# Optimization experiments

Measured on AMD Instinct MI355X. Metric: run time of the kernel, lower is better.

## Reference

```python
import jax, jax.numpy as jnp
import numpy as np

B, T, D = 2, 2048, 4096
H, KH, HD = 32, 8, 128          # n_heads, n_kv_heads, head_dim = D // H
WINDOW, NGLOBAL = 1024, 32      # sliding window size, global sink tokens
ROPE_BASE = 500000.0


def _rope_tables(seq_len, dim):
    inv_freq = 1.0 / (ROPE_BASE ** (np.arange(0, dim, 2, dtype=np.float64) / dim))
    freqs = np.outer(np.arange(seq_len, dtype=np.float64), inv_freq)
    emb = np.concatenate([freqs, freqs], axis=-1)  # [T, HD]
    cos = jnp.asarray(np.cos(emb), dtype=jnp.float32)[None, None]  # [1,1,T,HD]
    sin = jnp.asarray(np.sin(emb), dtype=jnp.float32)[None, None]
    return cos, sin


def _window_global_mask(seq_len, window, n_global):
    i = np.arange(seq_len)[:, None]  # query pos
    j = np.arange(seq_len)[None, :]  # key pos
    causal = j <= i
    local = j > (i - window)
    global_keys = j < n_global
    return jnp.asarray(causal & (local | global_keys))[None, None]  # [1,1,T,T] bool


def rotate_half(x):
    x1, x2 = jnp.split(x, 2, axis=-1)
    return jnp.concatenate([-x2, x1], axis=-1)


def setup_inputs() -> dict:
    key = jax.random.key(0)
    kx, kq, kk, kv, ko = jax.random.split(key, 5)
    s = 1.0 / np.sqrt(D)
    x = jax.random.normal(kx, (B, T, D), dtype=jnp.float32)
    # Linear weights stored [in, out] (y = x @ W), same math as torch's x @ W.T
    Wq = jax.random.normal(kq, (D, H * HD), dtype=jnp.float32) * s
    Wk = jax.random.normal(kk, (D, KH * HD), dtype=jnp.float32) * s
    Wv = jax.random.normal(kv, (D, KH * HD), dtype=jnp.float32) * s
    Wo = jax.random.normal(ko, (H * HD, D), dtype=jnp.float32) * s
    cos, sin = _rope_tables(T, HD)
    mask = _window_global_mask(T, WINDOW, NGLOBAL)
    return {"x": x, "Wq": Wq, "Wk": Wk, "Wv": Wv, "Wo": Wo,
            "cos": cos, "sin": sin, "mask": mask}


def reference(x, Wq, Wk, Wv, Wo, cos, sin, mask):
    Bx, Tx, Dx = x.shape
    q = (x @ Wq).reshape(Bx, Tx, H, HD).transpose(0, 2, 1, 3)   # [B,H,T,HD]
    k = (x @ Wk).reshape(Bx, Tx, KH, HD).transpose(0, 2, 1, 3)  # [B,KH,T,HD]
    v = (x @ Wv).reshape(Bx, Tx, KH, HD).transpose(0, 2, 1, 3)
    # RoPE
    q = q * cos + rotate_half(q) * sin
    k = k * cos + rotate_half(k) * sin
    # GQA: repeat_interleave KV heads to match query heads (faithful to source)
    factor = H // KH
    k = jnp.repeat(k, factor, axis=1)  # [B,H,T,HD]
    v = jnp.repeat(v, factor, axis=1)
    # SDPA with dense bool mask (True = attend), default scale 1/sqrt(HD)
    scale = 1.0 / np.sqrt(HD)
    scores = jnp.einsum('bhqd,bhkd->bhqk', q, k) * scale  # [B,H,T,T]
    scores = jnp.where(mask, scores, jnp.finfo(scores.dtype).min)
    attn = jax.nn.softmax(scores, axis=-1)
    out = jnp.einsum('bhqk,bhkd->bhqd', attn, v)
    out = out.transpose(0, 2, 1, 3).reshape(Bx, Tx, H * HD)
    return out @ Wo
```

## Files before the change

kernel.cpp:

```cpp
#include <hip/hip_runtime.h>
#include <stdint.h>

typedef unsigned short u16;
typedef __bf16 bf16x8 __attribute__((ext_vector_type(8)));
typedef float f32x4 __attribute__((ext_vector_type(4)));

#define D_MODEL 4096
#define T_SEQ   2048
#define B_SZ    2
#define NH      32
#define NKV     8
#define HDIM    128
#define WINDOW  1024
#define NGLOB   32
#define QSTR    6144

static constexpr float SCALE = 0.08838834764831845f;

__device__ __forceinline__ u16 f2b(float f) {
  __bf16 h = (__bf16)f;
  return __builtin_bit_cast(u16, h);
}
__device__ __forceinline__ float b2f(u16 u) {
  return (float)__builtin_bit_cast(__bf16, u);
}

__global__ __launch_bounds__(256) void convert_bf16_kernel(const float* __restrict__ in,
                                                           u16* __restrict__ outp, int n4) {
  int i = blockIdx.x * 256 + threadIdx.x;
  if (i >= n4) return;
  float4 v = ((const float4*)in)[i];
  ushort4 o;
  o.x = f2b(v.x); o.y = f2b(v.y); o.z = f2b(v.z); o.w = f2b(v.w);
  ((ushort4*)outp)[i] = o;
}

__global__ __launch_bounds__(256) void transpose_w_kernel(const float* __restrict__ W,
                                                          u16* __restrict__ Wt, int Kd, int Nd) {
  __shared__ float tile[32][33];
  int tx = threadIdx.x & 31, ty = threadIdx.x >> 5;
  int bx = blockIdx.x * 32;
  int by = blockIdx.y * 32;
#pragma unroll
  for (int i = 0; i < 4; ++i)
    tile[ty + i * 8][tx] = W[(size_t)(by + ty + i * 8) * Nd + bx + tx];
  __syncthreads();
#pragma unroll
  for (int i = 0; i < 4; ++i)
    Wt[(size_t)(bx + ty + i * 8) * Kd + by + tx] = f2b(tile[tx][ty + i * 8]);
}

__global__ __launch_bounds__(256) void transpose_v_kernel(const u16* __restrict__ in,
                                                          u16* __restrict__ outp) {
  __shared__ u16 tile[32][33];
  int tx = threadIdx.x & 31, ty = threadIdx.x >> 5;
  int x0 = blockIdx.x * 32;
  int t0 = blockIdx.y * 32;
  int b = blockIdx.z;
  const u16* src = in + (size_t)b * T_SEQ * QSTR;
  u16* dst = outp + (size_t)b * (NKV * HDIM) * T_SEQ;
#pragma unroll
  for (int i = 0; i < 4; ++i)
    tile[ty + i * 8][tx] = src[(size_t)(t0 + ty + i * 8) * QSTR + x0 + tx];
  __syncthreads();
#pragma unroll
  for (int i = 0; i < 4; ++i)
    dst[(size_t)(x0 + ty + i * 8) * T_SEQ + t0 + tx] = tile[tx][ty + i * 8];
}

template <typename CT>
__global__ __launch_bounds__(512, 2) void gemm256_kernel(const u16* __restrict__ A,
                                                         const u16* __restrict__ Bt,
                                                         CT* __restrict__ C,
                                                         int ldc, int K) {
  __shared__ u16 sh[65536];
  const int tid = threadIdx.x;
  const int wave = tid >> 6, lane = tid & 63;
  const int g = lane >> 4, li = lane & 15;
  const int wr = wave >> 2, wc = wave & 3;
  const int m0 = blockIdx.y * 256, n0 = blockIdx.x * 256;
  const int r0 = tid >> 3;
  const int cs = ((tid & 7) ^ ((tid >> 3) & 7)) << 3;
  const u16* pA = A + (size_t)(m0 + r0) * K + cs;
  const u16* pB = Bt + (size_t)(n0 + r0) * K + cs;
  const int sl0 = (g ^ (li & 7)) << 3;
  const int sl1 = ((4 + g) ^ (li & 7)) << 3;
  const int nT = K >> 6;

  f32x4 acc[8][4];
  f32x4 zz = {0.f, 0.f, 0.f, 0.f};
#pragma unroll
  for (int M = 0; M < 8; ++M)
#pragma unroll
    for (int n = 0; n < 4; ++n) acc[M][n] = zz;

  auto stage = [&](const u16* src0, int ts, int dstBase) {
#pragma unroll
    for (int i = 0; i < 2; ++i) {
      const u16* s = src0 + (size_t)(i * 64) * K + ts * 64;
      __builtin_amdgcn_global_load_lds((__attribute__((address_space(1))) void*)s,
                                       (__attribute__((address_space(3))) void*)(sh + dstBase + i * 4096 + wave * 512),
                                       16, 0, 0);
    }
  };

  stage(pA, 0, 0);
  stage(pA + (size_t)128 * K, 0, 8192);
  stage(pB, 0, 16384);
  stage(pB + (size_t)128 * K, 0, 24576);
  stage(pB, 1, 32768 + 16384);
  stage(pB + (size_t)128 * K, 1, 32768 + 24576);
  stage(pA, 1, 32768);
  asm volatile("s_waitcnt vmcnt(6)" ::: "memory");
  __builtin_amdgcn_s_barrier();

  bf16x8 afr[4][2], bfr[4][2];
  for (int t = 0; t < nT; ++t) {
    const int cur = t & 1;
    const int ab = cur * 32768, bb = ab + 16384;
    const int nb = (cur ^ 1) * 32768;
    const int tn1 = (t + 1 < nT) ? t + 1 : nT - 1;
    const int tn2 = (t + 2 < nT) ? t + 2 : nT - 1;
#pragma unroll
    for (int n = 0; n < 4; ++n) {
      int row = wc * 64 + n * 16 + li;
      bfr[n][0] = *(const bf16x8*)&sh[bb + row * 64 + sl0];
      bfr[n][1] = *(const bf16x8*)&sh[bb + row * 64 + sl1];
    }
#pragma unroll
    for (int m = 0; m < 4; ++m) {
      int row = wr * 128 + m * 16 + li;
      afr[m][0] = *(const bf16x8*)&sh[ab + row * 64 + sl0];
      afr[m][1] = *(const bf16x8*)&sh[ab + row * 64 + sl1];
    }
    stage(pA + (size_t)128 * K, tn1, nb + 8192);
    __builtin_amdgcn_s_barrier();
    asm volatile("s_waitcnt lgkmcnt(0)" ::: "memory");
    __builtin_amdgcn_sched_barrier(0);
    __builtin_amdgcn_s_setprio(1);
#pragma unroll
    for (int m = 0; m < 4; ++m)
#pragma unroll
      for (int n = 0; n < 2; ++n) {
        acc[m][n] = __builtin_amdgcn_mfma_f32_16x16x32_bf16(afr[m][0], bfr[n][0], acc[m][n], 0, 0, 0);
        acc[m][n] = __builtin_amdgcn_mfma_f32_16x16x32_bf16(afr[m][1], bfr[n][1], acc[m][n], 0, 0, 0);
      }
    __builtin_amdgcn_s_setprio(0);
    __builtin_amdgcn_s_barrier();
    stage(pB, tn2, bb);
    __builtin_amdgcn_s_barrier();
    __builtin_amdgcn_s_setprio(1);
#pragma unroll
    for (int m = 0; m < 4; ++m)
#pragma unroll
      for (int n = 2; n < 4; ++n) {
        acc[m][n] = __builtin_amdgcn_mfma_f32_16x16x32_bf16(afr[m][0], bfr[n][0], acc[m][n], 0, 0, 0);
        acc[m][n] = __builtin_amdgcn_mfma_f32_16x16x32_bf16(afr[m][1], bfr[n][1], acc[m][n], 0, 0, 0);
      }
    __builtin_amdgcn_s_setprio(0);
    __builtin_amdgcn_s_barrier();
#pragma unroll
    for (int m = 0; m < 4; ++m) {
      int row = wr * 128 + 64 + m * 16 + li;
      afr[m][0] = *(const bf16x8*)&sh[ab + row * 64 + sl0];
      afr[m][1] = *(const bf16x8*)&sh[ab + row * 64 + sl1];
    }
    stage(pB + (size_t)128 * K, tn2, bb + 8192);
    __builtin_amdgcn_s_barrier();
    asm volatile("s_waitcnt lgkmcnt(0)" ::: "memory");
    __builtin_amdgcn_sched_barrier(0);
    __builtin_amdgcn_s_setprio(1);
#pragma unroll
    for (int m = 0; m < 4; ++m)
#pragma unroll
      for (int n = 0; n < 2; ++n) {
        acc[4 + m][n] = __builtin_amdgcn_mfma_f32_16x16x32_bf16(afr[m][0], bfr[n][0], acc[4 + m][n], 0, 0, 0);
        acc[4 + m][n] = __builtin_amdgcn_mfma_f32_16x16x32_bf16(afr[m][1], bfr[n][1], acc[4 + m][n], 0, 0, 0);
      }
    __builtin_amdgcn_s_setprio(0);
    __builtin_amdgcn_s_barrier();
    stage(pA, tn2, ab);
    __builtin_amdgcn_s_barrier();
    __builtin_amdgcn_s_setprio(1);
#pragma unroll
    for (int m = 0; m < 4; ++m)
#pragma unroll
      for (int n = 2; n < 4; ++n) {
        acc[4 + m][n] = __builtin_amdgcn_mfma_f32_16x16x32_bf16(afr[m][0], bfr[n][0], acc[4 + m][n], 0, 0, 0);
        acc[4 + m][n] = __builtin_amdgcn_mfma_f32_16x16x32_bf16(afr[m][1], bfr[n][1], acc[4 + m][n], 0, 0, 0);
      }
    __builtin_amdgcn_s_setprio(0);
    asm volatile("s_waitcnt vmcnt(6)" ::: "memory");
    __builtin_amdgcn_s_barrier();
  }
#pragma unroll
  for (int M = 0; M < 8; ++M)
#pragma unroll
    for (int n = 0; n < 4; ++n)
#pragma unroll
      for (int r = 0; r < 4; ++r) {
        int row = m0 + wr * 128 + M * 16 + g * 4 + r;
        int col = n0 + wc * 64 + n * 16 + li;
        if constexpr (sizeof(CT) == 2)
          C[(size_t)row * ldc + col] = (CT)f2b(acc[M][n][r]);
        else
          C[(size_t)row * ldc + col] = acc[M][n][r];
      }
}

__global__ __launch_bounds__(512, 2) void gemm192_kernel(const u16* __restrict__ A,
                                                         const u16* __restrict__ Bt,
                                                         u16* __restrict__ C,
                                                         int ldc, int K) {
  __shared__ u16 sh[57344];
  const int tid = threadIdx.x;
  const int wave = tid >> 6, lane = tid & 63;
  const int g = lane >> 4, li = lane & 15;
  const int wr = wave >> 2, wc = wave & 3;
  const int m0 = blockIdx.y * 256, n0 = blockIdx.x * 192;
  const int r0 = tid >> 3;
  const int cs = ((tid & 7) ^ ((tid >> 3) & 7)) << 3;
  const u16* pA = A + (size_t)(m0 + r0) * K + cs;
  const u16* pB = Bt + (size_t)(n0 + r0) * K + cs;
  const int sl0 = (g ^ (li & 7)) << 3;
  const int sl1 = ((4 + g) ^ (li & 7)) << 3;
  const int nT = K >> 6;

  f32x4 acc[8][3];
  f32x4 zz = {0.f, 0.f, 0.f, 0.f};
#pragma unroll
  for (int M = 0; M < 8; ++M)
#pragma unroll
    for (int n = 0; n < 3; ++n) acc[M][n] = zz;

  auto stage64 = [&](const u16* src0, int ts, int dstU16) {
    __builtin_amdgcn_global_load_lds(
        (__attribute__((address_space(1))) void*)(src0 + (size_t)ts * 64),
        (__attribute__((address_space(3))) void*)(sh + dstU16 + wave * 512), 16, 0, 0);
  };

#pragma unroll
  for (int u = 0; u < 4; ++u) stage64(pA + (size_t)(u * 64) * K, 0, u * 4096);
#pragma unroll
  for (int u = 0; u < 3; ++u) stage64(pB + (size_t)(u * 64) * K, 0, 16384 + u * 4096);
#pragma unroll
  for (int u = 0; u < 4; ++u) stage64(pA + (size_t)(u * 64) * K, 1, 28672 + u * 4096);
#pragma unroll
  for (int u = 0; u < 3; ++u) stage64(pB + (size_t)(u * 64) * K, 1, 28672 + 16384 + u * 4096);
  asm volatile("s_waitcnt vmcnt(7)" ::: "memory");
  __builtin_amdgcn_s_barrier();

  bf16x8 afr[4][2], bfr[3][2];
  for (int t = 0; t < nT; ++t) {
    const int ab = (t & 1) * 28672, bb = ab + 16384;
    const int tn2 = (t + 2 < nT) ? t + 2 : nT - 1;
#pragma unroll
    for (int n = 0; n < 3; ++n) {
      int row = wc * 48 + n * 16 + li;
      bfr[n][0] = *(const bf16x8*)&sh[bb + row * 64 + sl0];
      bfr[n][1] = *(const bf16x8*)&sh[bb + row * 64 + sl1];
    }
#pragma unroll
    for (int m = 0; m < 4; ++m) {
      int row = wr * 128 + m * 16 + li;
      afr[m][0] = *(const bf16x8*)&sh[ab + row * 64 + sl0];
      afr[m][1] = *(const bf16x8*)&sh[ab + row * 64 + sl1];
    }
    __builtin_amdgcn_s_barrier();
    asm volatile("s_waitcnt lgkmcnt(0)" ::: "memory");
    __builtin_amdgcn_sched_barrier(0);
    __builtin_amdgcn_s_setprio(1);
#pragma unroll
    for (int m = 0; m < 4; ++m)
#pragma unroll
      for (int n = 0; n < 2; ++n) {
        acc[m][n] = __builtin_amdgcn_mfma_f32_16x16x32_bf16(afr[m][0], bfr[n][0], acc[m][n], 0, 0, 0);
        acc[m][n] = __builtin_amdgcn_mfma_f32_16x16x32_bf16(afr[m][1], bfr[n][1], acc[m][n], 0, 0, 0);
      }
    __builtin_amdgcn_s_setprio(0);
    __builtin_amdgcn_s_barrier();
    stage64(pB, tn2, bb);
    stage64(pB + (size_t)64 * K, tn2, bb + 4096);
    stage64(pA, tn2, ab);
    __builtin_amdgcn_s_barrier();
    __builtin_amdgcn_s_setprio(1);
#pragma unroll
    for (int m = 0; m < 4; ++m) {
      acc[m][2] = __builtin_amdgcn_mfma_f32_16x16x32_bf16(afr[m][0], bfr[2][0], acc[m][2], 0, 0, 0);
      acc[m][2] = __builtin_amdgcn_mfma_f32_16x16x32_bf16(afr[m][1], bfr[2][1], acc[m][2], 0, 0, 0);
    }
    __builtin_amdgcn_s_setprio(0);
    __builtin_amdgcn_s_barrier();
#pragma unroll
    for (int m = 0; m < 4; ++m) {
      int row = wr * 128 + 64 + m * 16 + li;
      afr[m][0] = *(const bf16x8*)&sh[ab + row * 64 + sl0];
      afr[m][1] = *(const bf16x8*)&sh[ab + row * 64 + sl1];
    }
    stage64(pB + (size_t)128 * K, tn2, bb + 8192);
    stage64(pA + (size_t)128 * K, tn2, ab + 8192);
    __builtin_amdgcn_s_barrier();
    asm volatile("s_waitcnt lgkmcnt(0)" ::: "memory");
    __builtin_amdgcn_sched_barrier(0);
    __builtin_amdgcn_s_setprio(1);
#pragma unroll
    for (int m = 0; m < 4; ++m)
#pragma unroll
      for (int n = 0; n < 2; ++n) {
        acc[4 + m][n] = __builtin_amdgcn_mfma_f32_16x16x32_bf16(afr[m][0], bfr[n][0], acc[4 + m][n], 0, 0, 0);
        acc[4 + m][n] = __builtin_amdgcn_mfma_f32_16x16x32_bf16(afr[m][1], bfr[n][1], acc[4 + m][n], 0, 0, 0);
      }
    __builtin_amdgcn_s_setprio(0);
    __builtin_amdgcn_s_barrier();
    stage64(pA + (size_t)64 * K, tn2, ab + 4096);
    stage64(pA + (size_t)192 * K, tn2, ab + 12288);
    __builtin_amdgcn_s_barrier();
    __builtin_amdgcn_s_setprio(1);
#pragma unroll
    for (int m = 0; m < 4; ++m) {
      acc[4 + m][2] = __builtin_amdgcn_mfma_f32_16x16x32_bf16(afr[m][0], bfr[2][0], acc[4 + m][2], 0, 0, 0);
      acc[4 + m][2] = __builtin_amdgcn_mfma_f32_16x16x32_bf16(afr[m][1], bfr[2][1], acc[4 + m][2], 0, 0, 0);
    }
    __builtin_amdgcn_s_setprio(0);
    asm volatile("s_waitcnt vmcnt(7)" ::: "memory");
    __builtin_amdgcn_s_barrier();
  }
#pragma unroll
  for (int M = 0; M < 8; ++M)
#pragma unroll
    for (int n = 0; n < 3; ++n)
#pragma unroll
      for (int r = 0; r < 4; ++r) {
        int row = m0 + wr * 128 + M * 16 + g * 4 + r;
        int col = n0 + wc * 48 + n * 16 + li;
        C[(size_t)row * ldc + col] = f2b(acc[M][n][r]);
      }
}

__global__ __launch_bounds__(256) void rope_kernel(u16* __restrict__ qkv,
                                                   const float* __restrict__ cosp,
                                                   const float* __restrict__ sinp) {
  int idx = blockIdx.x * 256 + threadIdx.x;
  int d8 = idx & 7;
  int rest = idx >> 3;
  int hh = rest % (NH + NKV);
  int bt = rest / (NH + NKV);
  if (bt >= B_SZ * T_SEQ) return;
  int tok = bt & (T_SEQ - 1);
  int d0 = d8 * 8;
  const float4* cp = (const float4*)(cosp + (size_t)tok * HDIM + d0);
  const float4* sp = (const float4*)(sinp + (size_t)tok * HDIM + d0);
  float4 cA = cp[0], cB = cp[1];
  float4 sA = sp[0], sB = sp[1];
  float cc[8] = {cA.x, cA.y, cA.z, cA.w, cB.x, cB.y, cB.z, cB.w};
  float ss[8] = {sA.x, sA.y, sA.z, sA.w, sB.x, sB.y, sB.z, sB.w};
  u16* base = qkv + (size_t)bt * QSTR + hh * HDIM;
  bf16x8 v1 = *(const bf16x8*)(base + d0);
  bf16x8 v2 = *(const bf16x8*)(base + d0 + 64);
  bf16x8 o1, o2;
#pragma unroll
  for (int j = 0; j < 8; ++j) {
    float xa = (float)v1[j], xb = (float)v2[j];
    o1[j] = (__bf16)(xa * cc[j] - xb * ss[j]);
    o2[j] = (__bf16)(xb * cc[j] + xa * ss[j]);
  }
  *(bf16x8*)(base + d0) = o1;
  *(bf16x8*)(base + d0 + 64) = o2;
}

__global__ __launch_bounds__(256) void attn_kernel(const u16* __restrict__ qp,
                                                   const u16* __restrict__ kp,
                                                   const u16* __restrict__ vtp,
                                                   u16* __restrict__ ctx) {
  __shared__ u16 Kt[64 * 128];
  __shared__ u16 Vt[128 * 64];
  __shared__ u16 Pl[4][16 * 64];
  int tid = threadIdx.x;
  int w = tid >> 6, lane = tid & 63;
  int g = lane >> 4, li = lane & 15;
  int i0 = blockIdx.x * 64;
  int h = blockIdx.y, b = blockIdx.z;
  int kh = h >> 2;
  f32x4 zz = {0.f, 0.f, 0.f, 0.f};

  bf16x8 qf[4];
  size_t qrow = (size_t)(b * T_SEQ + i0 + w * 16 + li) * QSTR + h * HDIM;
#pragma unroll
  for (int c = 0; c < 4; ++c) qf[c] = *(const bf16x8*)(qp + qrow + c * 32 + g * 8);

  f32x4 o[8];
#pragma unroll
  for (int f = 0; f < 8; ++f) o[f] = zz;
  float m_s[4] = {-1e30f, -1e30f, -1e30f, -1e30f};
  float l_s[4] = {0.f, 0.f, 0.f, 0.f};

  int jmax = i0 + 63;
  for (int j0 = 0; j0 <= jmax; j0 += 64) {
    if (!((j0 < NGLOB) || (j0 + 63 > i0 - WINDOW))) continue;
    __syncthreads();
#pragma unroll
    for (int i = 0; i < 4; ++i) {
      int o8 = tid + 256 * i;
      int krow = o8 >> 4, kch = o8 & 15;
      size_t gk = (size_t)(b * T_SEQ + j0 + krow) * QSTR + kh * HDIM + kch * 8;
      *(bf16x8*)&Kt[(krow * 128 + kch * 8) ^ ((krow & 7) << 3)] = *(const bf16x8*)(kp + gk);
      int vrow = o8 >> 3, vch = o8 & 7;
      size_t gv = ((size_t)(b * NKV + kh) * HDIM + vrow) * T_SEQ + j0 + vch * 8;
      *(bf16x8*)&Vt[(vrow * 64 + vch * 8) ^ ((vrow & 7) << 3)] = *(const bf16x8*)(vtp + gv);
    }
    __syncthreads();

    f32x4 s[4];
#pragma unroll
    for (int kb = 0; kb < 4; ++kb) s[kb] = zz;
#pragma unroll
    for (int c = 0; c < 4; ++c) {
      int hd0 = c * 32 + g * 8;
#pragma unroll
      for (int kb = 0; kb < 4; ++kb) {
        int key = kb * 16 + li;
        bf16x8 kf = *(const bf16x8*)&Kt[(key * 128 + hd0) ^ ((key & 7) << 3)];
        s[kb] = __builtin_amdgcn_mfma_f32_16x16x32_bf16(qf[c], kf, s[kb], 0, 0, 0);
      }
    }

    float corr[4];
#pragma unroll
    for (int r = 0; r < 4; ++r) {
      int irow = i0 + w * 16 + g * 4 + r;
      float x[4];
#pragma unroll
      for (int kb = 0; kb < 4; ++kb) {
        int j = j0 + kb * 16 + li;
        float xx = s[kb][r] * SCALE;
        bool vm = (j <= irow) && ((j > irow - WINDOW) || (j < NGLOB));
        x[kb] = vm ? xx : -1e30f;
      }
      float mt = fmaxf(fmaxf(x[0], x[1]), fmaxf(x[2], x[3]));
#pragma unroll
      for (int dd = 1; dd < 16; dd <<= 1) mt = fmaxf(mt, __shfl_xor(mt, dd, 64));
      float mn = fmaxf(m_s[r], mt);
      corr[r] = __expf(m_s[r] - mn);
      m_s[r] = mn;
      float rs = 0.f;
      int prow = g * 4 + r;
#pragma unroll
      for (int kb = 0; kb < 4; ++kb) {
        x[kb] = __expf(x[kb] - mn);
        rs += x[kb];
        Pl[w][(prow * 64 + kb * 16 + li) ^ ((prow & 7) << 3)] = f2b(x[kb]);
      }
#pragma unroll
      for (int dd = 1; dd < 16; dd <<= 1) rs += __shfl_xor(rs, dd, 64);
      l_s[r] = l_s[r] * corr[r] + rs;
    }
#pragma unroll
    for (int f = 0; f < 8; ++f) {
      o[f][0] *= corr[0]; o[f][1] *= corr[1];
      o[f][2] *= corr[2]; o[f][3] *= corr[3];
    }

    bf16x8 pa0 = *(const bf16x8*)&Pl[w][(li * 64 + 0 + g * 8) ^ ((li & 7) << 3)];
    bf16x8 pa1 = *(const bf16x8*)&Pl[w][(li * 64 + 32 + g * 8) ^ ((li & 7) << 3)];

#pragma unroll
    for (int f = 0; f < 8; ++f) {
      int hd = f * 16 + li;
      bf16x8 v0 = *(const bf16x8*)&Vt[(hd * 64 + 0 + g * 8) ^ ((li & 7) << 3)];
      bf16x8 v1 = *(const bf16x8*)&Vt[(hd * 64 + 32 + g * 8) ^ ((li & 7) << 3)];
      o[f] = __builtin_amdgcn_mfma_f32_16x16x32_bf16(pa0, v0, o[f], 0, 0, 0);
      o[f] = __builtin_amdgcn_mfma_f32_16x16x32_bf16(pa1, v1, o[f], 0, 0, 0);
    }
  }

#pragma unroll
  for (int f = 0; f < 8; ++f)
#pragma unroll
    for (int r = 0; r < 4; ++r) {
      size_t orow = (size_t)(b * T_SEQ + i0 + w * 16 + g * 4 + r) * (NH * HDIM) + h * HDIM + f * 16 + li;
      ctx[orow] = f2b(o[f][r] / l_s[r]);
    }
}

extern "C" void kernel_launch(void* const* d_in, const int* in_sizes, int n_in,
                              void* d_out, int out_size, void* d_ws, size_t ws_size,
                              hipStream_t stream) {
  const float* x    = (const float*)d_in[0];
  const float* Wq   = (const float*)d_in[1];
  const float* Wk   = (const float*)d_in[2];
  const float* Wv   = (const float*)d_in[3];
  const float* Wo   = (const float*)d_in[4];
  const float* cosp = (const float*)d_in[5];
  const float* sinp = (const float*)d_in[6];

  char* ws = (char*)d_ws;
  u16* xb     = (u16*)(ws + 0ull);
  u16* Wqkvt  = (u16*)(ws + 33554432ull);
  u16* Wot    = (u16*)(ws + 83886080ull);
  u16* qkv    = (u16*)(ws + 117440512ull);
  u16* ctx    = xb;
  u16* vT     = Wqkvt;

  convert_bf16_kernel<<<16384, 256, 0, stream>>>(x, xb, 4194304);
  transpose_w_kernel<<<dim3(128, 128), 256, 0, stream>>>(Wq, Wqkvt, 4096, 4096);
  transpose_w_kernel<<<dim3(32, 128), 256, 0, stream>>>(Wk, Wqkvt + (size_t)4096 * 4096, 4096, 1024);
  transpose_w_kernel<<<dim3(32, 128), 256, 0, stream>>>(Wv, Wqkvt + (size_t)5120 * 4096, 4096, 1024);
  transpose_w_kernel<<<dim3(128, 128), 256, 0, stream>>>(Wo, Wot, 4096, 4096);

  gemm192_kernel<<<dim3(32, 16), 512, 0, stream>>>(xb, Wqkvt, qkv, QSTR, 4096);

  transpose_v_kernel<<<dim3(32, 64, 2), 256, 0, stream>>>(qkv + 5120, vT);

  rope_kernel<<<5120, 256, 0, stream>>>(qkv, cosp, sinp);

  attn_kernel<<<dim3(32, 32, 2), 256, 0, stream>>>(qkv, qkv + 4096, vT, ctx);

  gemm256_kernel<float><<<dim3(16, 16), 512, 0, stream>>>(ctx, Wot, (float*)d_out, 4096, 4096);
}
```

Baseline: 577.4 us.

## Enlarge attention query tile, load K/V directly to LDS, transpose score MFMA

The attention block grows from 64 to 128 query rows with 8 waves, so each K/V tile staged in shared memory serves twice as many queries. K/V tiles are copied with global_load_lds direct-to-LDS transfers, with the swizzle moved into the global address. The QK^T MFMA operands are swapped so each lane owns one query row, which turns the row-max and row-sum reductions into two cross-group shuffles. The softmax scale is folded into Q during RoPE, which adds an extra bf16 rounding of scaled Q. Larger blocks cut the grid in half and may process more fully masked rows near the diagonal.

```diff
diff --git a/kernel.cpp b/kernel.cpp
--- a/kernel.cpp
+++ b/kernel.cpp
@@ -20,9 +20,6 @@
 __device__ __forceinline__ u16 f2b(float f) {
   __bf16 h = (__bf16)f;
   return __builtin_bit_cast(u16, h);
-}
-__device__ __forceinline__ float b2f(u16 u) {
-  return (float)__builtin_bit_cast(__bf16, u);
 }
 
 __global__ __launch_bounds__(256) void convert_bf16_kernel(const float* __restrict__ in,
@@ -354,6 +351,7 @@
   float4 sA = sp[0], sB = sp[1];
   float cc[8] = {cA.x, cA.y, cA.z, cA.w, cB.x, cB.y, cB.z, cB.w};
   float ss[8] = {sA.x, sA.y, sA.z, sA.w, sB.x, sB.y, sB.z, sB.w};
+  float scl = (hh < NH) ? SCALE : 1.0f;
   u16* base = qkv + (size_t)bt * QSTR + hh * HDIM;
   bf16x8 v1 = *(const bf16x8*)(base + d0);
   bf16x8 v2 = *(const bf16x8*)(base + d0 + 64);
@@ -361,24 +359,24 @@
 #pragma unroll
   for (int j = 0; j < 8; ++j) {
     float xa = (float)v1[j], xb = (float)v2[j];
-    o1[j] = (__bf16)(xa * cc[j] - xb * ss[j]);
-    o2[j] = (__bf16)(xb * cc[j] + xa * ss[j]);
+    o1[j] = (__bf16)((xa * cc[j] - xb * ss[j]) * scl);
+    o2[j] = (__bf16)((xb * cc[j] + xa * ss[j]) * scl);
   }
   *(bf16x8*)(base + d0) = o1;
   *(bf16x8*)(base + d0 + 64) = o2;
 }
 
-__global__ __launch_bounds__(256) void attn_kernel(const u16* __restrict__ qp,
+__global__ __launch_bounds__(512) void attn_kernel(const u16* __restrict__ qp,
                                                    const u16* __restrict__ kp,
                                                    const u16* __restrict__ vtp,
                                                    u16* __restrict__ ctx) {
   __shared__ u16 Kt[64 * 128];
   __shared__ u16 Vt[128 * 64];
-  __shared__ u16 Pl[4][16 * 64];
+  __shared__ u16 Pl[8][16 * 64];
   int tid = threadIdx.x;
   int w = tid >> 6, lane = tid & 63;
   int g = lane >> 4, li = lane & 15;
-  int i0 = blockIdx.x * 64;
+  int i0 = blockIdx.x * 128;
   int h = blockIdx.y, b = blockIdx.z;
   int kh = h >> 2;
   f32x4 zz = {0.f, 0.f, 0.f, 0.f};
@@ -391,22 +389,26 @@
   f32x4 o[8];
 #pragma unroll
   for (int f = 0; f < 8; ++f) o[f] = zz;
-  float m_s[4] = {-1e30f, -1e30f, -1e30f, -1e30f};
-  float l_s[4] = {0.f, 0.f, 0.f, 0.f};
-
-  int jmax = i0 + 63;
+  float m_s = -1e30f, l_s = 0.f;
+  const int irow = i0 + w * 16 + li;
+
+  int jmax = i0 + 127;
   for (int j0 = 0; j0 <= jmax; j0 += 64) {
     if (!((j0 < NGLOB) || (j0 + 63 > i0 - WINDOW))) continue;
     __syncthreads();
 #pragma unroll
-    for (int i = 0; i < 4; ++i) {
-      int o8 = tid + 256 * i;
+    for (int i = 0; i < 2; ++i) {
+      int o8 = tid + 512 * i;
       int krow = o8 >> 4, kch = o8 & 15;
-      size_t gk = (size_t)(b * T_SEQ + j0 + krow) * QSTR + kh * HDIM + kch * 8;
-      *(bf16x8*)&Kt[(krow * 128 + kch * 8) ^ ((krow & 7) << 3)] = *(const bf16x8*)(kp + gk);
+      size_t gk = (size_t)(b * T_SEQ + j0 + krow) * QSTR + kh * HDIM + (kch ^ (krow & 7)) * 8;
+      __builtin_amdgcn_global_load_lds((__attribute__((address_space(1))) void*)(kp + gk),
+                                       (__attribute__((address_space(3))) void*)(Kt + o8 * 8),
+                                       16, 0, 0);
       int vrow = o8 >> 3, vch = o8 & 7;
-      size_t gv = ((size_t)(b * NKV + kh) * HDIM + vrow) * T_SEQ + j0 + vch * 8;
-      *(bf16x8*)&Vt[(vrow * 64 + vch * 8) ^ ((vrow & 7) << 3)] = *(const bf16x8*)(vtp + gv);
+      size_t gv = ((size_t)(b * NKV + kh) * HDIM + vrow) * T_SEQ + j0 + (vch ^ (vrow & 7)) * 8;
+      __builtin_amdgcn_global_load_lds((__attribute__((address_space(1))) void*)(vtp + gv),
+                                       (__attribute__((address_space(3))) void*)(Vt + o8 * 8),
+                                       16, 0, 0);
     }
     __syncthreads();
 
@@ -420,44 +422,50 @@
       for (int kb = 0; kb < 4; ++kb) {
         int key = kb * 16 + li;
         bf16x8 kf = *(const bf16x8*)&Kt[(key * 128 + hd0) ^ ((key & 7) << 3)];
-        s[kb] = __builtin_amdgcn_mfma_f32_16x16x32_bf16(qf[c], kf, s[kb], 0, 0, 0);
-      }
-    }
-
-    float corr[4];
-#pragma unroll
-    for (int r = 0; r < 4; ++r) {
-      int irow = i0 + w * 16 + g * 4 + r;
-      float x[4];
-#pragma unroll
-      for (int kb = 0; kb < 4; ++kb) {
-        int j = j0 + kb * 16 + li;
-        float xx = s[kb][r] * SCALE;
+        s[kb] = __builtin_amdgcn_mfma_f32_16x16x32_bf16(kf, qf[c], s[kb], 0, 0, 0);
+      }
+    }
+
+    float x[4][4];
+    float mt = -1e30f;
+#pragma unroll
+    for (int kb = 0; kb < 4; ++kb)
+#pragma unroll
+      for (int r = 0; r < 4; ++r) {
+        int j = j0 + kb * 16 + g * 4 + r;
         bool vm = (j <= irow) && ((j > irow - WINDOW) || (j < NGLOB));
-        x[kb] = vm ? xx : -1e30f;
-      }
-      float mt = fmaxf(fmaxf(x[0], x[1]), fmaxf(x[2], x[3]));
-#pragma unroll
-      for (int dd = 1; dd < 16; dd <<= 1) mt = fmaxf(mt, __shfl_xor(mt, dd, 64));
-      float mn = fmaxf(m_s[r], mt);
-      corr[r] = __expf(m_s[r] - mn);
-      m_s[r] = mn;
-      float rs = 0.f;
-      int prow = g * 4 + r;
-#pragma unroll
-      for (int kb = 0; kb < 4; ++kb) {
-        x[kb] = __expf(x[kb] - mn);
-        rs += x[kb];
-        Pl[w][(prow * 64 + kb * 16 + li) ^ ((prow & 7) << 3)] = f2b(x[kb]);
-      }
-#pragma unroll
-      for (int dd = 1; dd < 16; dd <<= 1) rs += __shfl_xor(rs, dd, 64);
-      l_s[r] = l_s[r] * corr[r] + rs;
-    }
+        float xx = vm ? s[kb][r] : -1e30f;
+        x[kb][r] = xx;
+        mt = fmaxf(mt, xx);
+      }
+    mt = fmaxf(mt, __shfl_xor(mt, 16, 64));
+    mt = fmaxf(mt, __shfl_xor(mt, 32, 64));
+    float mn = fmaxf(m_s, mt);
+    float corr = __expf(m_s - mn);
+    m_s = mn;
+    float rs = 0.f;
+#pragma unroll
+    for (int kb = 0; kb < 4; ++kb) {
+      ushort4 pk;
+#pragma unroll
+      for (int r = 0; r < 4; ++r) {
+        float p = __expf(x[kb][r] - mn);
+        rs += p;
+        ((u16*)&pk)[r] = f2b(p);
+      }
+      *(ushort4*)&Pl[w][(li * 64 + kb * 16 + g * 4) ^ ((li & 7) << 3)] = pk;
+    }
+    rs += __shfl_xor(rs, 16, 64);
+    rs += __shfl_xor(rs, 32, 64);
+    l_s = l_s * corr + rs;
+
+    float c4[4];
+#pragma unroll
+    for (int r = 0; r < 4; ++r) c4[r] = __shfl(corr, g * 4 + r, 16);
 #pragma unroll
     for (int f = 0; f < 8; ++f) {
-      o[f][0] *= corr[0]; o[f][1] *= corr[1];
-      o[f][2] *= corr[2]; o[f][3] *= corr[3];
+      o[f][0] *= c4[0]; o[f][1] *= c4[1];
+      o[f][2] *= c4[2]; o[f][3] *= c4[3];
     }
 
     bf16x8 pa0 = *(const bf16x8*)&Pl[w][(li * 64 + 0 + g * 8) ^ ((li & 7) << 3)];
@@ -473,12 +481,15 @@
     }
   }
 
+  float l4[4];
+#pragma unroll
+  for (int r = 0; r < 4; ++r) l4[r] = __shfl(l_s, g * 4 + r, 16);
 #pragma unroll
   for (int f = 0; f < 8; ++f)
 #pragma unroll
     for (int r = 0; r < 4; ++r) {
       size_t orow = (size_t)(b * T_SEQ + i0 + w * 16 + g * 4 + r) * (NH * HDIM) + h * HDIM + f * 16 + li;
-      ctx[orow] = f2b(o[f][r] / l_s[r]);
+      ctx[orow] = f2b(o[f][r] / l4[r]);
     }
 }
 
@@ -513,7 +524,7 @@
 
   rope_kernel<<<5120, 256, 0, stream>>>(qkv, cosp, sinp);
 
-  attn_kernel<<<dim3(32, 32, 2), 256, 0, stream>>>(qkv, qkv + 4096, vT, ctx);
+  attn_kernel<<<dim3(16, 32, 2), 512, 0, stream>>>(qkv, qkv + 4096, vT, ctx);
 
   gemm256_kernel<float><<<dim3(16, 16), 512, 0, stream>>>(ctx, Wot, (float*)d_out, 4096, 4096);
 }
```

New measurement: 553.4 us. 1.04x faster.
